# Kernel tuning notes

Measured on AMD Instinct MI355X. Metric: run time of the kernel, lower is better.

Reference implementation:

```python
import jax, jax.numpy as jnp
import numpy as np
from jax import lax

B, C, H, W = 8, 512, 48, 48
E = 512          # embed_dim (== in_channels, required by GLoR fusion channel math)
P = 128          # ContextBlock planes = int(512*0.25)
NC = 2           # num_classes; also used (buggily, but faithfully) as BGAM threshold
TOPK_RATIO = 0.1


def conv1x1(x, w, b=None):
    # w: [out, in]
    y = jnp.einsum('bchw,oc->bohw', x, w)
    if b is not None:
        y = y + b[None, :, None, None]
    return y


def conv3x3(x, w, b):
    y = lax.conv_general_dilated(x, w, (1, 1), 'SAME',
                                 dimension_numbers=('NCHW', 'OIHW', 'NCHW'))
    return y + b[None, :, None, None]


def dwconv3x3(x, w):
    # depthwise: w [C,1,3,3], feature_group_count=C
    return lax.conv_general_dilated(x, w, (1, 1), 'SAME',
                                    dimension_numbers=('NCHW', 'OIHW', 'NCHW'),
                                    feature_group_count=x.shape[1])


def bn_eval(x, g, b):
    # eval-mode BatchNorm2d, running_mean=0, running_var=1, eps=1e-5
    scale = g / jnp.sqrt(1.0 + 1e-5)
    return x * scale[None, :, None, None] + b[None, :, None, None]


def chan_mlp(c, w1, b1, g, bl, w2, b2):
    # ContextBlock channel transform: 1x1 conv -> LayerNorm([P,1,1]) -> ReLU -> 1x1 conv, on [B,C] vectors
    h = c @ w1.T + b1                                  # [B,P]
    mu = h.mean(-1, keepdims=True)
    var = jnp.var(h, axis=-1, keepdims=True)
    h = (h - mu) / jnp.sqrt(var + 1e-5) * g + bl
    h = jax.nn.relu(h)
    return h @ w2.T + b2                               # [B,C]


def cos_self(t):
    # torch F.cosine_similarity(t, t, dim=1): dot/(max(n,eps)*max(n,eps)), eps=1e-8
    nrm2 = jnp.sum(t * t, axis=1)                      # [B,H,W]
    n = jnp.maximum(jnp.sqrt(nrm2), 1e-8)
    return nrm2 / (n * n)


def setup_inputs() -> dict:
    key = jax.random.key(0)
    ks = iter(jax.random.split(key, 64))
    def nrm(shape, scale):
        return (jax.random.normal(next(ks), shape) * scale).astype(jnp.float32)
    def gma(n):
        return (1.0 + 0.05 * jax.random.normal(next(ks), (n,))).astype(jnp.float32)
    def bta(n):
        return (0.05 * jax.random.normal(next(ks), (n,))).astype(jnp.float32)
    sC = 1.0 / np.sqrt(C)
    return dict(
        x=jax.random.normal(next(ks), (B, C, H, W), jnp.float32),
        # GLoR local ConvBranch
        lb_w1=nrm((E, C), sC), lb_g1=gma(E), lb_b1=bta(E),
        lb_w2=nrm((E, 1, 3, 3), 1.0 / 3.0), lb_g2=gma(E), lb_b2=bta(E),
        lb_w3=nrm((E, E), 1.0 / np.sqrt(E)), lb_g3=gma(E), lb_b3=bta(E),
        # GLoR ContextBlock (att pooling, channel_add + channel_mul)
        cm_w=nrm((1, C), sC), cm_b=bta(1),
        ca_w1=nrm((P, C), sC), ca_b1=bta(P), ca_lg=gma(P), ca_lb=bta(P),
        ca_w2=nrm((C, P), 1.0 / np.sqrt(P)), ca_b2=bta(C),
        cmu_w1=nrm((P, C), sC), cmu_b1=bta(P), cmu_lg=gma(P), cmu_lb=bta(P),
        cmu_w2=nrm((C, P), 1.0 / np.sqrt(P)), cmu_b2=bta(C),
        fu_w=nrm((E, 2 * E), 1.0 / np.sqrt(2 * E)), fu_b=bta(E),
        # heads
        sh_w=nrm((NC, E), 1.0 / np.sqrt(E)), sh_b=bta(NC),
        bh_w=nrm((2, E), 1.0 / np.sqrt(E)), bh_b=bta(2),
        # ReverseAttention
        ra_w1=nrm((2, 2, 3, 3), 1.0 / np.sqrt(18)), ra_b1=bta(2), ra_g1=gma(2), ra_bb1=bta(2),
        ra_w2=nrm((2, 2, 3, 3), 1.0 / np.sqrt(18)), ra_b2=bta(2), ra_g2=gma(2), ra_bb2=bta(2),
        # AGCR (all bias=False)
        q_w=nrm((E // 4, E), 1.0 / np.sqrt(E)), k_w=nrm((E // 4, E), 1.0 / np.sqrt(E)),
        v_w=nrm((E, E), 1.0 / np.sqrt(E)), fin_w=nrm((E, 2 * E), 1.0 / np.sqrt(2 * E)),
    )


def reference(x, lb_w1, lb_g1, lb_b1, lb_w2, lb_g2, lb_b2, lb_w3, lb_g3, lb_b3,
              cm_w, cm_b, ca_w1, ca_b1, ca_lg, ca_lb, ca_w2, ca_b2,
              cmu_w1, cmu_b1, cmu_lg, cmu_lb, cmu_w2, cmu_b2, fu_w, fu_b,
              sh_w, sh_b, bh_w, bh_b,
              ra_w1, ra_b1, ra_g1, ra_bb1, ra_w2, ra_b2, ra_g2, ra_bb2,
              q_w, k_w, v_w, fin_w):
    b_, c_, h_, w_ = x.shape
    N = h_ * w_
    # ---- GLoR: local ConvBranch ----
    t = jax.nn.relu(bn_eval(conv1x1(x, lb_w1), lb_g1, lb_b1))
    t = jax.nn.relu(bn_eval(dwconv3x3(t, lb_w2), lb_g2, lb_b2))
    local = bn_eval(conv1x1(t, lb_w3), lb_g3, lb_b3)
    # ---- GLoR: ContextBlock (att pooling) ----
    xf = x.reshape(b_, c_, N)
    mask = (conv1x1(x, cm_w, cm_b)).reshape(b_, 1, N)
    mask = jax.nn.softmax(mask, axis=2)
    ctx = jnp.einsum('bcn,bn->bc', xf, mask[:, 0, :])              # [B,C]
    mul = jax.nn.sigmoid(chan_mlp(ctx, cmu_w1, cmu_b1, cmu_lg, cmu_lb, cmu_w2, cmu_b2))
    add = chan_mlp(ctx, ca_w1, ca_b1, ca_lg, ca_lb, ca_w2, ca_b2)
    glob = x * mul[:, :, None, None] + add[:, :, None, None]
    gx = conv1x1(jnp.concatenate([local, glob], axis=1), fu_w, fu_b)  # [B,E,H,W]
    # ---- heads ----
    sem = conv1x1(gx, sh_w, sh_b)                                   # [B,NC,H,W]
    bdl = conv1x1(gx, bh_w, bh_b)                                   # [B,2,H,W]
    # ---- ReverseAttention(boundary_logits, sigmoid(boundary_logits)) ----
    wx = bdl * (1.0 - jax.nn.sigmoid(bdl))
    r = jax.nn.relu(bn_eval(conv3x3(wx, ra_w1, ra_b1), ra_g1, ra_bb1))
    r = jax.nn.relu(bn_eval(conv3x3(r, ra_w2, ra_b2), ra_g2, ra_bb2))
    # ---- BGAM (threshold = num_classes, faithful to source) ----
    thr = jnp.float32(NC)
    st = (cos_self(sem) > thr).astype(x.dtype)
    bt = (cos_self(r) > thr).astype(x.dtype)
    region = ((1.0 - st) * (1.0 - bt))[:, None]                     # [B,1,H,W]
    # ---- AGCR custom attention ----
    k_num = int(N * TOPK_RATIO)
    q = conv1x1(gx, q_w).reshape(b_, -1, N)                         # [B,E/4,N]
    kk = conv1x1(gx, k_w).reshape(b_, -1, N)
    v = conv1x1(gx, v_w).reshape(b_, E, N)
    attn = jnp.einsum('bdm,bdn->bmn', q, kk) / jnp.sqrt(jnp.float32(q.shape[1]))
    aw = jax.nn.softmax(attn, axis=-1)                              # [B,N,N]
    topv, _ = lax.top_k(aw, k_num)
    soft = topv.mean(-1)                                            # [B,N]
    aw = aw * soft[:, None, :]
    # bmm(value, aw^T).mean(-1) == value @ aw.mean(rows)
    col_mean = aw.mean(axis=1)                                      # [B,N]
    ctx2 = jnp.einsum('bcn,bn->bc', v, col_mean)                    # [B,E]
    ctx2 = jnp.broadcast_to(ctx2[:, :, None, None], gx.shape)
    refined = jnp.concatenate([gx, ctx2 * region], axis=1)          # [B,2E,H,W]
    return conv1x1(refined, fin_w)                                  # [B,E,H,W]
```

## Files before the change

### kernel.cpp

```cpp
#include <hip/hip_runtime.h>
#include <math.h>

#define NPIX 2304
#define NCH  512
#define NB   8
#define KNUM 230

typedef unsigned short u16;
typedef __attribute__((ext_vector_type(8))) short short8v;
typedef __attribute__((ext_vector_type(4))) float float4v;

__device__ __forceinline__ float bf2f(u16 u) {
    union { unsigned v; float f; } x; x.v = ((unsigned)u) << 16; return x.f;
}
__device__ __forceinline__ u16 f2bf(float f) {
    union { float f; unsigned v; } x; x.f = f;
    unsigned r = x.v + 0x7FFFu + ((x.v >> 16) & 1u);
    return (u16)(r >> 16);
}

__device__ __forceinline__ float waveSum(float v) {
    #pragma unroll
    for (int o = 32; o > 0; o >>= 1) v += __shfl_down(v, o);
    return v;
}
__device__ __forceinline__ float blockSum256(float v, float* sc4) {
    v = waveSum(v);
    __syncthreads();
    if ((threadIdx.x & 63) == 0) sc4[threadIdx.x >> 6] = v;
    __syncthreads();
    return sc4[0] + sc4[1] + sc4[2] + sc4[3];
}
__device__ __forceinline__ float waveMaxF(float v) {
    #pragma unroll
    for (int o = 32; o > 0; o >>= 1) v = fmaxf(v, __shfl_down(v, o));
    return v;
}
__device__ __forceinline__ float blockMax256(float v, float* sc4) {
    v = waveMaxF(v);
    __syncthreads();
    if ((threadIdx.x & 63) == 0) sc4[threadIdx.x >> 6] = v;
    __syncthreads();
    return fmaxf(fmaxf(sc4[0], sc4[1]), fmaxf(sc4[2], sc4[3]));
}

__device__ __forceinline__ void gl_lds16(const u16* g, u16* l) {
    __builtin_amdgcn_global_load_lds(
        reinterpret_cast<const unsigned __attribute__((address_space(1)))*>(
            reinterpret_cast<uintptr_t>(g)),
        reinterpret_cast<unsigned __attribute__((address_space(3)))*>(
            reinterpret_cast<uintptr_t>(l)),
        16, 0, 0);
}

__global__ __launch_bounds__(256, 3) void mfma_gemm(
    const u16* __restrict__ A, int ldA, long sA,
    const u16* __restrict__ B0, const u16* __restrict__ B1, int ldB, long sB,
    void* __restrict__ outp, int ldO, long sO,
    const float* __restrict__ scaleR, const float* __restrict__ biasR,
    const float* __restrict__ biasC, int ldbc,
    const float* __restrict__ biasRB, int ldrb,
    int K, float alpha, int flags)
{
    __shared__ u16 lA[128 * 64];
    __shared__ u16 lB[128 * 64];
    const int t  = threadIdx.x;
    const int w  = t >> 6, l = t & 63;
    const int wR = w >> 1, wC = w & 1;
    const int lg = l >> 4, lr = l & 15, l7 = l & 7;
    const int b   = blockIdx.z;
    const int Cl0 = blockIdx.x * 128;
    const int R0  = blockIdx.y * 128;
    const u16* Ab  = A + (size_t)b * sA;
    const u16* B0b = B0 + (size_t)b * sB;
    const u16* B1b = B1 ? B1 + (size_t)b * sB : nullptr;

    float4v acc[4][4];
    const float4v zero = {0.f, 0.f, 0.f, 0.f};
    #pragma unroll
    for (int i = 0; i < 4; ++i)
        #pragma unroll
        for (int j = 0; j < 4; ++j) acc[i][j] = zero;

    const int sr = t >> 3;
    const int sp = t & 7;

    for (int k0 = 0; k0 < K; k0 += 64) {
        const u16* Bsrc = B0b; int kb = k0;
        if (B1b && k0 >= 512) { Bsrc = B1b; kb = k0 - 512; }
        #pragma unroll
        for (int i = 0; i < 4; ++i) {
            const int r  = i * 32 + sr;
            const int ca = sp ^ (r & 7);
            gl_lds16(Ab   + (size_t)(R0  + r) * ldA + (k0 + ca * 8), &lA[i * 2048 + t * 8]);
            gl_lds16(Bsrc + (size_t)(Cl0 + r) * ldB + (kb + ca * 8), &lB[i * 2048 + t * 8]);
        }
        __syncthreads();
        #pragma unroll
        for (int kk = 0; kk < 2; ++kk) {
            short8v af[4], bfv[4];
            const int p = (kk * 4 + lg) ^ l7;
            #pragma unroll
            for (int mt = 0; mt < 4; ++mt) {
                const int rA = wR * 64 + mt * 16 + lr;
                af[mt]  = *reinterpret_cast<const short8v*>(&lA[rA * 64 + p * 8]);
                const int rB = wC * 64 + mt * 16 + lr;
                bfv[mt] = *reinterpret_cast<const short8v*>(&lB[rB * 64 + p * 8]);
            }
            #pragma unroll
            for (int mt = 0; mt < 4; ++mt)
                #pragma unroll
                for (int nt = 0; nt < 4; ++nt)
                    acc[mt][nt] = __builtin_amdgcn_mfma_f32_16x16x32_bf16(
                        af[mt], bfv[nt], acc[mt][nt], 0, 0, 0);
        }
        __syncthreads();
    }

    const bool relu = (flags & 1), f32o = (flags & 2);
    #pragma unroll
    for (int nt = 0; nt < 4; ++nt) {
        const int Cl = Cl0 + wC * 64 + nt * 16 + lr;
        const float bc = biasC ? biasC[(size_t)b * ldbc + Cl] : 0.f;
        #pragma unroll
        for (int mt = 0; mt < 4; ++mt) {
            const int Rb = R0 + wR * 64 + mt * 16 + lg * 4;
            float4 scv = scaleR ? *reinterpret_cast<const float4*>(&scaleR[Rb])
                                : make_float4(1.f, 1.f, 1.f, 1.f);
            float4 bv  = biasR  ? *reinterpret_cast<const float4*>(&biasR[Rb])
                                : make_float4(0.f, 0.f, 0.f, 0.f);
            float4 rbv = biasRB ? *reinterpret_cast<const float4*>(&biasRB[(size_t)b * ldrb + Rb])
                                : make_float4(0.f, 0.f, 0.f, 0.f);
            float vals[4];
            #pragma unroll
            for (int j = 0; j < 4; ++j) {
                const float sc = alpha * ((&scv.x)[j]);
                float v = acc[mt][nt][j] * sc + (&bv.x)[j] + bc + (&rbv.x)[j];
                if (relu) v = fmaxf(v, 0.f);
                vals[j] = v;
            }
            if (f32o) {
                float* op = (float*)outp + (size_t)b * sO + (size_t)Cl * ldO + Rb;
                *reinterpret_cast<float4*>(op) = make_float4(vals[0], vals[1], vals[2], vals[3]);
            } else {
                ushort4 u;
                u.x = f2bf(vals[0]); u.y = f2bf(vals[1]);
                u.z = f2bf(vals[2]); u.w = f2bf(vals[3]);
                u16* op = (u16*)outp + (size_t)b * sO + (size_t)Cl * ldO + Rb;
                *reinterpret_cast<ushort4*>(op) = u;
            }
        }
    }
}

__global__ __launch_bounds__(256) void transpose_cvt_ml(
    const float* __restrict__ x, const float* __restrict__ cmw,
    u16* __restrict__ xb, float* __restrict__ logits)
{
    __shared__ float tile[64][65];
    const int t = threadIdx.x;
    const int n0 = blockIdx.x * 64, c0 = blockIdx.y * 64, b = blockIdx.z;
    const int tr = t >> 4, tc4 = (t & 15) * 4;
    #pragma unroll
    for (int i = 0; i < 4; ++i) {
        const int cc = tr + i * 16;
        float4 v = *reinterpret_cast<const float4*>(
            x + ((size_t)(b * NCH + c0 + cc)) * NPIX + n0 + tc4);
        tile[cc][tc4 + 0] = v.x; tile[cc][tc4 + 1] = v.y;
        tile[cc][tc4 + 2] = v.z; tile[cc][tc4 + 3] = v.w;
    }
    __syncthreads();
    #pragma unroll
    for (int i = 0; i < 4; ++i) {
        const int nn = tr + i * 16;
        ushort4 u;
        u.x = f2bf(tile[tc4 + 0][nn]); u.y = f2bf(tile[tc4 + 1][nn]);
        u.z = f2bf(tile[tc4 + 2][nn]); u.w = f2bf(tile[tc4 + 3][nn]);
        *reinterpret_cast<ushort4*>(xb + ((size_t)b * NPIX + n0 + nn) * NCH + c0 + tc4) = u;
    }
    const int nl = t >> 2, q = t & 3;
    float s = 0.f;
    #pragma unroll
    for (int k = 0; k < 16; ++k) {
        const int cc = q * 16 + k;
        s = fmaf(tile[cc][nl], cmw[c0 + cc], s);
    }
    s += __shfl_xor(s, 1);
    s += __shfl_xor(s, 2);
    if (q == 0) atomicAdd(&logits[(size_t)b * NPIX + n0 + nl], s);
}

__global__ __launch_bounds__(256) void transpose_w3(
    const float* __restrict__ w3, const float* __restrict__ g3, u16* __restrict__ w3t)
{
    __shared__ float tile[64][65];
    const int t = threadIdx.x;
    const int k0 = blockIdx.x * 64, c0 = blockIdx.y * 64;
    const int tr = t >> 4, tc4 = (t & 15) * 4;
    #pragma unroll
    for (int i = 0; i < 4; ++i) {
        const int cc = tr + i * 16;
        const float s = g3[c0 + cc] * 0.99999500003749978f;
        float4 v = *reinterpret_cast<const float4*>(&w3[(size_t)(c0 + cc) * 512 + k0 + tc4]);
        tile[cc][tc4 + 0] = v.x * s; tile[cc][tc4 + 1] = v.y * s;
        tile[cc][tc4 + 2] = v.z * s; tile[cc][tc4 + 3] = v.w * s;
    }
    __syncthreads();
    #pragma unroll
    for (int i = 0; i < 4; ++i) {
        const int kk = tr + i * 16;
        ushort4 u;
        u.x = f2bf(tile[tc4 + 0][kk]); u.y = f2bf(tile[tc4 + 1][kk]);
        u.z = f2bf(tile[tc4 + 2][kk]); u.w = f2bf(tile[tc4 + 3][kk]);
        *reinterpret_cast<ushort4*>(&w3t[(size_t)(k0 + kk) * 512 + c0 + tc4]) = u;
    }
}

__device__ __forceinline__ void cvt4(const float* s, u16* d, int i) {
    float4 v = reinterpret_cast<const float4*>(s)[i];
    ushort4 u; u.x = f2bf(v.x); u.y = f2bf(v.y); u.z = f2bf(v.z); u.w = f2bf(v.w);
    reinterpret_cast<ushort4*>(d)[i] = u;
}
__global__ __launch_bounds__(256) void prep_weights(
    const float* __restrict__ w1, const float* __restrict__ fu,
    const float* __restrict__ fin, const float* __restrict__ qw,
    const float* __restrict__ kw, const float* __restrict__ vw,
    const float* __restrict__ dww, const float* __restrict__ dwg,
    u16* __restrict__ w1b, u16* __restrict__ fuwb, u16* __restrict__ finwb,
    u16* __restrict__ qkvwb, float* __restrict__ wfold)
{
    const int i = blockIdx.x * 256 + threadIdx.x;
    if (i < 65536)            cvt4(w1, w1b, i);
    else if (i < 196608)      cvt4(fu, fuwb, i - 65536);
    else if (i < 327680)      cvt4(fin, finwb, i - 196608);
    else if (i < 344064)      cvt4(qw, qkvwb, i - 327680);
    else if (i < 360448)      cvt4(kw, qkvwb + 128 * 512, i - 344064);
    else if (i < 425984)      cvt4(vw, qkvwb + 256 * 512, i - 360448);
    else if (i < 425984 + 4608) {
        const int j = i - 425984;
        const int c = j / 9, tap = j % 9;
        wfold[tap * NCH + c] = dww[j] * dwg[c] * 0.99999500003749978f;
    }
}

__global__ __launch_bounds__(256) void dwconv_k(
    const u16* __restrict__ t1, const float* __restrict__ wf,
    const float* __restrict__ b2, u16* __restrict__ t2)
{
    const int idx = blockIdx.x * 256 + threadIdx.x;
    const int cq = idx & 127;
    const int n  = (idx >> 7) % NPIX;
    const int b  = (idx >> 7) / NPIX;
    const int c  = cq * 4;
    const int y = n / 48, x = n % 48;
    float s0 = 0.f, s1 = 0.f, s2 = 0.f, s3 = 0.f;
    #pragma unroll
    for (int dy = -1; dy <= 1; ++dy) {
        const int yy = y + dy;
        if (yy < 0 || yy >= 48) continue;
        #pragma unroll
        for (int dx = -1; dx <= 1; ++dx) {
            const int xx = x + dx;
            if (xx < 0 || xx >= 48) continue;
            ushort4 tv = *reinterpret_cast<const ushort4*>(
                &t1[((size_t)b * NPIX + yy * 48 + xx) * NCH + c]);
            float4 wv = *reinterpret_cast<const float4*>(
                &wf[((dy + 1) * 3 + dx + 1) * NCH + c]);
            s0 = fmaf(bf2f(tv.x), wv.x, s0); s1 = fmaf(bf2f(tv.y), wv.y, s1);
            s2 = fmaf(bf2f(tv.z), wv.z, s2); s3 = fmaf(bf2f(tv.w), wv.w, s3);
        }
    }
    float4 bb = *reinterpret_cast<const float4*>(&b2[c]);
    ushort4 o;
    o.x = f2bf(fmaxf(s0 + bb.x, 0.f)); o.y = f2bf(fmaxf(s1 + bb.y, 0.f));
    o.z = f2bf(fmaxf(s2 + bb.z, 0.f)); o.w = f2bf(fmaxf(s3 + bb.w, 0.f));
    *reinterpret_cast<ushort4*>(&t2[((size_t)b * NPIX + n) * NCH + c]) = o;
}

__global__ __launch_bounds__(256) void softmax_mask(
    const float* __restrict__ logits, float* __restrict__ mask)
{
    __shared__ float sc[4];
    const int b = blockIdx.x, t = threadIdx.x;
    const float* lr = logits + (size_t)b * NPIX;
    float mx = -3.4e38f;
    for (int i = t; i < NPIX; i += 256) mx = fmaxf(mx, lr[i]);
    mx = blockMax256(mx, sc);
    float s = 0.f;
    for (int i = t; i < NPIX; i += 256) s += __expf(lr[i] - mx);
    s = blockSum256(s, sc);
    const float inv = 1.0f / s;
    for (int i = t; i < NPIX; i += 256) mask[(size_t)b * NPIX + i] = __expf(lr[i] - mx) * inv;
}

__global__ __launch_bounds__(512) void ctx_pool_k(
    const u16* __restrict__ xb, const float* __restrict__ mask, float* __restrict__ ctx)
{
    const int c = threadIdx.x, b = blockIdx.y;
    const int nn0 = blockIdx.x * 128;
    float s = 0.f;
    for (int n = nn0; n < nn0 + 128; ++n)
        s = fmaf(bf2f(xb[((size_t)b * NPIX + n) * NCH + c]), mask[(size_t)b * NPIX + n], s);
    atomicAdd(&ctx[b * NCH + c], s);
}

__global__ __launch_bounds__(256) void chan_h(
    const float* __restrict__ ctxv,
    const float* __restrict__ mw1, const float* __restrict__ mb1,
    const float* __restrict__ aw1, const float* __restrict__ ab1,
    float* __restrict__ hnb)
{
    const int w = threadIdx.x >> 6, l = threadIdx.x & 63;
    const int gid = blockIdx.x * 4 + w;
    const int path = gid >> 10;
    const int rem  = gid & 1023;
    const int h = rem >> 3, b = rem & 7;
    const float* W1 = path ? aw1 : mw1;
    const float* B1 = path ? ab1 : mb1;
    const float4 wa = *reinterpret_cast<const float4*>(&W1[h * 512 + l * 8]);
    const float4 wb = *reinterpret_cast<const float4*>(&W1[h * 512 + l * 8 + 4]);
    const float4 ca = *reinterpret_cast<const float4*>(&ctxv[b * 512 + l * 8]);
    const float4 cb = *reinterpret_cast<const float4*>(&ctxv[b * 512 + l * 8 + 4]);
    float s = wa.x * ca.x + wa.y * ca.y + wa.z * ca.z + wa.w * ca.w
            + wb.x * cb.x + wb.y * cb.y + wb.z * cb.z + wb.w * cb.w;
    s = waveSum(s);
    if (l == 0) hnb[(path * 8 + b) * 128 + h] = s + B1[h];
}

__global__ __launch_bounds__(128) void chan_ln(
    const float* __restrict__ mlg, const float* __restrict__ mlb,
    const float* __restrict__ alg, const float* __restrict__ alb,
    float* __restrict__ hnb)
{
    __shared__ float sc[2];
    const int path = blockIdx.x, b = blockIdx.y, t = threadIdx.x;
    float* hp = hnb + (path * 8 + b) * 128;
    const float v = hp[t];
    float s1 = waveSum(v);
    if ((t & 63) == 0) sc[t >> 6] = s1;
    __syncthreads();
    const float mu = (sc[0] + sc[1]) * (1.0f / 128.0f);
    const float d = v - mu;
    float s2 = waveSum(d * d);
    __syncthreads();
    if ((t & 63) == 0) sc[t >> 6] = s2;
    __syncthreads();
    const float var = (sc[0] + sc[1]) * (1.0f / 128.0f);
    const float* LG = path ? alg : mlg;
    const float* LB = path ? alb : mlb;
    hp[t] = fmaxf(d / sqrtf(var + 1e-5f) * LG[t] + LB[t], 0.f);
}

__global__ __launch_bounds__(128) void chan_o(
    const float* __restrict__ hnb,
    const float* __restrict__ mw2, const float* __restrict__ mb2,
    const float* __restrict__ aw2, const float* __restrict__ ab2,
    float* __restrict__ mulo, float* __restrict__ addo)
{
    __shared__ float hs[128];
    const int oc = blockIdx.x, path = blockIdx.y, b = blockIdx.z;
    const int t = threadIdx.x;
    hs[t] = hnb[(path * 8 + b) * 128 + t];
    __syncthreads();
    const int o = oc * 128 + t;
    const float* W2 = path ? aw2 : mw2;
    float s = (path ? ab2 : mb2)[o];
    #pragma unroll
    for (int p = 0; p < 128; p += 4) {
        const float4 wv = *reinterpret_cast<const float4*>(&W2[o * 128 + p]);
        s += wv.x * hs[p] + wv.y * hs[p + 1] + wv.z * hs[p + 2] + wv.w * hs[p + 3];
    }
    if (path == 0) mulo[b * 512 + o] = 1.0f / (1.0f + __expf(-s));
    else           addo[b * 512 + o] = s;
}

__global__ __launch_bounds__(256) void scale_wglob(
    const float* __restrict__ fuw, const float* __restrict__ mulv, u16* __restrict__ wf)
{
    const int idx = blockIdx.x * 256 + threadIdx.x;
    const int cq = idx & 127;
    const int o  = (idx >> 7) & 511;
    const int b  = idx >> 16;
    const int c  = cq * 4;
    float4 w = *reinterpret_cast<const float4*>(&fuw[(size_t)o * 1024 + 512 + c]);
    float4 m = *reinterpret_cast<const float4*>(&mulv[b * 512 + c]);
    ushort4 u;
    u.x = f2bf(w.x * m.x); u.y = f2bf(w.y * m.y);
    u.z = f2bf(w.z * m.z); u.w = f2bf(w.w * m.w);
    *reinterpret_cast<ushort4*>(&wf[(size_t)b * 524288 + (size_t)o * 1024 + 512 + c]) = u;
}

__global__ __launch_bounds__(256) void fuse_bias(
    const float* __restrict__ fuw, const float* __restrict__ fub,
    const float* __restrict__ b3, const float* __restrict__ addv, float* __restrict__ fb)
{
    const int o = blockIdx.x * 256 + threadIdx.x;
    const int b = blockIdx.y;
    const float* wr = fuw + (size_t)o * 1024;
    float s = fub[o];
    for (int c = 0; c < 512; c += 4) {
        float4 w1 = *reinterpret_cast<const float4*>(&wr[c]);
        float4 bv = *reinterpret_cast<const float4*>(&b3[c]);
        float4 w2 = *reinterpret_cast<const float4*>(&wr[512 + c]);
        float4 av = *reinterpret_cast<const float4*>(&addv[b * 512 + c]);
        s += w1.x * bv.x + w1.y * bv.y + w1.z * bv.z + w1.w * bv.w
           + w2.x * av.x + w2.y * av.y + w2.z * av.z + w2.w * av.w;
    }
    fb[b * 512 + o] = s;
}

__global__ __launch_bounds__(256) void softmax_topk_wave(
    const u16* __restrict__ p, float* __restrict__ mxo,
    float* __restrict__ invSo, float* __restrict__ softo)
{
    const int w = threadIdx.x >> 6, l = threadIdx.x & 63;
    const int r = blockIdx.x * 4 + w;
    const int bc = blockIdx.y;
    const u16* pr = p + ((size_t)bc * NPIX + r) * NPIX;
    const uint4* p16 = reinterpret_cast<const uint4*>(pr);
    uint4 q0 = p16[l], q1 = p16[64 + l], q2 = p16[128 + l], q3 = p16[192 + l];
    uint2 q4 = reinterpret_cast<const uint2*>(pr)[512 + l];
    unsigned uw[18] = {q0.x, q0.y, q0.z, q0.w, q1.x, q1.y, q1.z, q1.w,
                       q2.x, q2.y, q2.z, q2.w, q3.x, q3.y, q3.z, q3.w,
                       q4.x, q4.y};
    unsigned km[36];
    #pragma unroll
    for (int i = 0; i < 18; ++i) {
        const unsigned v = uw[i];
        const unsigned m = ((v >> 15) & 0x10001u) * 0x7FFFu + 0x80008000u;
        const unsigned s = v ^ m;
        km[2 * i]     = s & 0xFFFFu;
        km[2 * i + 1] = s >> 16;
    }
    unsigned kmax = km[0];
    #pragma unroll
    for (int i = 1; i < 36; ++i) kmax = max(kmax, km[i]);
    #pragma unroll
    for (int o = 32; o > 0; o >>= 1) kmax = max(kmax, (unsigned)__shfl_xor((int)kmax, o));
    const unsigned mxbits = (kmax & 0x8000u) ? (kmax ^ 0x8000u) : (kmax ^ 0xFFFFu);
    const float mx = bf2f((u16)mxbits);
    unsigned kt = 0u;
    for (int bit = 15; bit >= 0; --bit) {
        const unsigned cand = kt | (1u << bit);
        int c = 0;
        #pragma unroll
        for (int i = 0; i < 36; ++i)
            c += (int)__popcll(__ballot(km[i] >= cand));
        if (c >= KNUM) kt = cand;
    }
    const unsigned tbits = (kt & 0x8000u) ? (kt ^ 0x8000u) : (kt ^ 0xFFFFu);
    const float te = __expf(bf2f((u16)tbits) - mx);
    float S = 0.f, ss = 0.f; int a = 0;
    #pragma unroll
    for (int i = 0; i < 36; ++i) {
        const unsigned bb = (km[i] & 0x8000u) ? (km[i] ^ 0x8000u) : (km[i] ^ 0xFFFFu);
        const float e = __expf(bf2f((u16)bb) - mx);
        S += e;
        const bool gt = km[i] > kt;
        if (gt) ss += e;
        a += (int)__popcll(__ballot(gt));
    }
    #pragma unroll
    for (int o = 32; o > 0; o >>= 1) { S += __shfl_xor(S, o); ss += __shfl_xor(ss, o); }
    if (l == 0) {
        const size_t gi = (size_t)bc * NPIX + r;
        mxo[gi] = mx; invSo[gi] = 1.0f / S;
        softo[gi] = (ss + (float)(KNUM - a) * te) / (S * (float)KNUM);
    }
}

__global__ __launch_bounds__(256) void colsum_k(
    const u16* __restrict__ p, const float* __restrict__ mxo,
    const float* __restrict__ invSo, float* __restrict__ colsum)
{
    const int j = blockIdx.x * 256 + threadIdx.x;
    const int ic0 = blockIdx.y * 72;
    const int bc = blockIdx.z;
    const float* mxr = mxo + (size_t)bc * NPIX;
    const float* isr = invSo + (size_t)bc * NPIX;
    const u16* pb = p + (size_t)bc * NPIX * NPIX;
    float s = 0.f;
    #pragma unroll 4
    for (int i = ic0; i < ic0 + 72; ++i)
        s += __expf(bf2f(pb[(size_t)i * NPIX + j]) - mxr[i]) * isr[i];
    atomicAdd(&colsum[(size_t)bc * NPIX + j], s);
}

__global__ __launch_bounds__(512) void ctx2_pool_k(
    const u16* __restrict__ qkv, const float* __restrict__ colsum,
    const float* __restrict__ soft, float* __restrict__ ctx2)
{
    const int c = threadIdx.x, b = blockIdx.y;
    const int nn0 = blockIdx.x * 128;
    float s = 0.f;
    for (int n = nn0; n < nn0 + 128; ++n) {
        const float wgt = colsum[(size_t)b * NPIX + n] * soft[(size_t)b * NPIX + n];
        s = fmaf(bf2f(qkv[((size_t)b * NPIX + n) * 768 + 256 + c]), wgt, s);
    }
    atomicAdd(&ctx2[b * NCH + c], s * (1.0f / (float)NPIX));
}

__global__ __launch_bounds__(256) void compute_z(
    const float* __restrict__ finw, const float* __restrict__ ctx2, float* __restrict__ z)
{
    const int o = blockIdx.x * 256 + threadIdx.x;
    const int b = blockIdx.y;
    const float* c2 = ctx2 + b * NCH;
    const float* wr = finw + (size_t)o * 1024 + 512;
    float s = 0.f;
    for (int c = 0; c < NCH; ++c) s = fmaf(wr[c], c2[c], s);
    z[b * NCH + o] = s;
}

extern "C" void kernel_launch(void* const* d_in, const int* in_sizes, int n_in,
                              void* d_out, int out_size, void* d_ws, size_t ws_size,
                              hipStream_t stream)
{
    (void)in_sizes; (void)n_in; (void)out_size; (void)ws_size;
    const float* x      = (const float*)d_in[0];
    const float* lb_w1  = (const float*)d_in[1];
    const float* lb_g1  = (const float*)d_in[2];
    const float* lb_b1  = (const float*)d_in[3];
    const float* lb_w2  = (const float*)d_in[4];
    const float* lb_g2  = (const float*)d_in[5];
    const float* lb_b2  = (const float*)d_in[6];
    const float* lb_w3  = (const float*)d_in[7];
    const float* lb_g3  = (const float*)d_in[8];
    const float* lb_b3  = (const float*)d_in[9];
    const float* cm_w   = (const float*)d_in[10];
    const float* ca_w1  = (const float*)d_in[12];
    const float* ca_b1  = (const float*)d_in[13];
    const float* ca_lg  = (const float*)d_in[14];
    const float* ca_lb  = (const float*)d_in[15];
    const float* ca_w2  = (const float*)d_in[16];
    const float* ca_b2  = (const float*)d_in[17];
    const float* cmu_w1 = (const float*)d_in[18];
    const float* cmu_b1 = (const float*)d_in[19];
    const float* cmu_lg = (const float*)d_in[20];
    const float* cmu_lb = (const float*)d_in[21];
    const float* cmu_w2 = (const float*)d_in[22];
    const float* cmu_b2 = (const float*)d_in[23];
    const float* fu_w   = (const float*)d_in[24];
    const float* fu_b   = (const float*)d_in[25];
    const float* q_w    = (const float*)d_in[38];
    const float* k_w    = (const float*)d_in[39];
    const float* v_w    = (const float*)d_in[40];
    const float* fin_w  = (const float*)d_in[41];

    char* W = (char*)d_ws;
    const size_t SZ_ACT = (size_t)NB * NPIX * NCH * 2;
    u16* xb   = (u16*)(W);
    u16* bufA = (u16*)(W + SZ_ACT);
    u16* bufB = (u16*)(W + 2 * SZ_ACT);
    u16* gx   = (u16*)(W + 3 * SZ_ACT);
    u16* qkv  = (u16*)(W + 4 * SZ_ACT);
    u16* wfused = qkv;
    u16* pbuf = (u16*)(W + 4 * SZ_ACT + (size_t)NB * NPIX * 768 * 2);
    char* SM = (char*)(pbuf + (size_t)NB * NPIX * NPIX);
    float* logits = (float*)SM; SM += (size_t)NB * NPIX * 4;
    float* colsum = (float*)SM; SM += (size_t)NB * NPIX * 4;
    float* ctxb   = (float*)SM; SM += (size_t)NB * NCH * 4;
    float* ctx2b  = (float*)SM; SM += (size_t)NB * NCH * 4;
    float* maskb  = (float*)SM; SM += (size_t)NB * NPIX * 4;
    float* mxb    = (float*)SM; SM += (size_t)NB * NPIX * 4;
    float* invSb  = (float*)SM; SM += (size_t)NB * NPIX * 4;
    float* softb  = (float*)SM; SM += (size_t)NB * NPIX * 4;
    float* mulb   = (float*)SM; SM += (size_t)NB * NCH * 4;
    float* addb   = (float*)SM; SM += (size_t)NB * NCH * 4;
    float* zbuf   = (float*)SM; SM += (size_t)NB * NCH * 4;
    float* fbias  = (float*)SM; SM += (size_t)NB * NCH * 4;
    float* hnb    = (float*)SM; SM += (size_t)2 * NB * 128 * 4;
    float* wfold  = (float*)SM; SM += (size_t)9 * NCH * 4;
    u16* w1b   = (u16*)SM; SM += (size_t)512 * 512 * 2;
    u16* fuwb  = (u16*)SM; SM += (size_t)512 * 1024 * 2;
    u16* finwb = (u16*)SM; SM += (size_t)512 * 1024 * 2;
    u16* qkvwb = (u16*)SM; SM += (size_t)768 * 512 * 2;
    u16* w3t   = (u16*)SM; SM += (size_t)512 * 512 * 2;

    const float invs  = 0.99999500003749978f;
    const float rs128 = 0.08838834764831845f;
    const long SACT = (long)NPIX * NCH;

    hipMemsetAsync(logits, 0,
        ((size_t)2 * NB * NPIX + (size_t)2 * NB * NCH) * 4, stream);
    prep_weights<<<1683, 256, 0, stream>>>(lb_w1, fu_w, fin_w, q_w, k_w, v_w,
        lb_w2, lb_g2, w1b, fuwb, finwb, qkvwb, wfold);
    transpose_cvt_ml<<<dim3(36, 8, 8), 256, 0, stream>>>(x, cm_w, xb, logits);
    transpose_w3<<<dim3(8, 8), 256, 0, stream>>>(lb_w3, lb_g3, w3t);

    mfma_gemm<<<dim3(4, 4, 8), 256, 0, stream>>>(w3t, 512, 0, fuwb, nullptr, 1024, 0,
        wfused, 1024, 524288, nullptr, nullptr, nullptr, 0, nullptr, 0, 512, 1.0f, 0);

    mfma_gemm<<<dim3(18, 4, 8), 256, 0, stream>>>(w1b, 512, 0, xb, nullptr, 512, SACT,
        bufA, 512, SACT, lb_g1, lb_b1, nullptr, 0, nullptr, 0, 512, invs, 1);
    dwconv_k<<<9216, 256, 0, stream>>>(bufA, wfold, lb_b2, bufB);
    softmax_mask<<<8, 256, 0, stream>>>(logits, maskb);
    ctx_pool_k<<<dim3(18, 8), 512, 0, stream>>>(xb, maskb, ctxb);
    chan_h<<<512, 256, 0, stream>>>(ctxb, cmu_w1, cmu_b1, ca_w1, ca_b1, hnb);
    chan_ln<<<dim3(2, 8), 128, 0, stream>>>(cmu_lg, cmu_lb, ca_lg, ca_lb, hnb);
    chan_o<<<dim3(4, 2, 8), 128, 0, stream>>>(hnb, cmu_w2, cmu_b2, ca_w2, ca_b2, mulb, addb);
    scale_wglob<<<2048, 256, 0, stream>>>(fu_w, mulb, wfused);
    fuse_bias<<<dim3(2, 8), 256, 0, stream>>>(fu_w, fu_b, lb_b3, addb, fbias);
    mfma_gemm<<<dim3(18, 4, 8), 256, 0, stream>>>(wfused, 1024, 524288, bufB, xb, 512, SACT,
        gx, 512, SACT, nullptr, nullptr, nullptr, 0, fbias, 512, 1024, 1.0f, 0);
    mfma_gemm<<<dim3(18, 6, 8), 256, 0, stream>>>(qkvwb, 512, 0, gx, nullptr, 512, SACT,
        qkv, 768, (long)NPIX * 768, nullptr, nullptr, nullptr, 0, nullptr, 0, 512, 1.0f, 0);
    mfma_gemm<<<dim3(18, 18, 8), 256, 0, stream>>>(qkv + 128, 768, (long)NPIX * 768,
        qkv, nullptr, 768, (long)NPIX * 768,
        pbuf, NPIX, (long)NPIX * NPIX, nullptr, nullptr, nullptr, 0, nullptr, 0,
        128, rs128, 0);
    softmax_topk_wave<<<dim3(576, 8), 256, 0, stream>>>(pbuf, mxb, invSb, softb);
    colsum_k<<<dim3(9, 32, 8), 256, 0, stream>>>(pbuf, mxb, invSb, colsum);
    ctx2_pool_k<<<dim3(18, 8), 512, 0, stream>>>(qkv, colsum, softb, ctx2b);
    compute_z<<<dim3(2, 8), 256, 0, stream>>>(fin_w, ctx2b, zbuf);
    mfma_gemm<<<dim3(4, 18, 8), 256, 0, stream>>>(gx, 512, SACT, finwb, nullptr, 1024, 0,
        d_out, NPIX, (long)NCH * NPIX, nullptr, nullptr, zbuf, 512, nullptr, 0,
        512, 1.0f, 2);
}
```

Before: 386.2 us.

## Fuse QK^T GEMM, softmax top-k and column sum into one LDS-resident kernel

Replaces the separate attention-score GEMM, the per-row softmax/top-k kernel and the column-sum kernel with one kernel. Each block computes a 16-row strip of scores with MFMA into shared memory, does the per-row max, top-k threshold and softmax statistics from LDS, then accumulates column sums with atomics. This removes the write and two re-reads of the full 8x2304x2304 bf16 score matrix in global memory and its workspace buffer. In exchange each block reloads K for the whole row strip from global/L2, uses about 74KB of LDS (limiting occupancy), and issues more atomics on colsum (144 contributions per column instead of 32).

New measurement: 467.2 us. 21.0% more time.

```diff
diff --git a/kernel.cpp b/kernel.cpp
--- a/kernel.cpp
+++ b/kernel.cpp
@@ -5,6 +5,7 @@
 #define NCH  512
 #define NB   8
 #define KNUM 230
+#define SROW 2312
 
 typedef unsigned short u16;
 typedef __attribute__((ext_vector_type(8))) short short8v;
@@ -409,81 +410,108 @@
     fb[b * 512 + o] = s;
 }
 
-__global__ __launch_bounds__(256) void softmax_topk_wave(
-    const u16* __restrict__ p, float* __restrict__ mxo,
-    float* __restrict__ invSo, float* __restrict__ softo)
-{
-    const int w = threadIdx.x >> 6, l = threadIdx.x & 63;
-    const int r = blockIdx.x * 4 + w;
-    const int bc = blockIdx.y;
-    const u16* pr = p + ((size_t)bc * NPIX + r) * NPIX;
-    const uint4* p16 = reinterpret_cast<const uint4*>(pr);
-    uint4 q0 = p16[l], q1 = p16[64 + l], q2 = p16[128 + l], q3 = p16[192 + l];
-    uint2 q4 = reinterpret_cast<const uint2*>(pr)[512 + l];
-    unsigned uw[18] = {q0.x, q0.y, q0.z, q0.w, q1.x, q1.y, q1.z, q1.w,
-                       q2.x, q2.y, q2.z, q2.w, q3.x, q3.y, q3.z, q3.w,
-                       q4.x, q4.y};
-    unsigned km[36];
-    #pragma unroll
-    for (int i = 0; i < 18; ++i) {
-        const unsigned v = uw[i];
-        const unsigned m = ((v >> 15) & 0x10001u) * 0x7FFFu + 0x80008000u;
-        const unsigned s = v ^ m;
-        km[2 * i]     = s & 0xFFFFu;
-        km[2 * i + 1] = s >> 16;
-    }
-    unsigned kmax = km[0];
-    #pragma unroll
-    for (int i = 1; i < 36; ++i) kmax = max(kmax, km[i]);
-    #pragma unroll
-    for (int o = 32; o > 0; o >>= 1) kmax = max(kmax, (unsigned)__shfl_xor((int)kmax, o));
-    const unsigned mxbits = (kmax & 0x8000u) ? (kmax ^ 0x8000u) : (kmax ^ 0xFFFFu);
-    const float mx = bf2f((u16)mxbits);
-    unsigned kt = 0u;
-    for (int bit = 15; bit >= 0; --bit) {
-        const unsigned cand = kt | (1u << bit);
-        int c = 0;
-        #pragma unroll
-        for (int i = 0; i < 36; ++i)
-            c += (int)__popcll(__ballot(km[i] >= cand));
-        if (c >= KNUM) kt = cand;
-    }
-    const unsigned tbits = (kt & 0x8000u) ? (kt ^ 0x8000u) : (kt ^ 0xFFFFu);
-    const float te = __expf(bf2f((u16)tbits) - mx);
-    float S = 0.f, ss = 0.f; int a = 0;
-    #pragma unroll
-    for (int i = 0; i < 36; ++i) {
-        const unsigned bb = (km[i] & 0x8000u) ? (km[i] ^ 0x8000u) : (km[i] ^ 0xFFFFu);
-        const float e = __expf(bf2f((u16)bb) - mx);
-        S += e;
-        const bool gt = km[i] > kt;
-        if (gt) ss += e;
-        a += (int)__popcll(__ballot(gt));
-    }
-    #pragma unroll
-    for (int o = 32; o > 0; o >>= 1) { S += __shfl_xor(S, o); ss += __shfl_xor(ss, o); }
-    if (l == 0) {
-        const size_t gi = (size_t)bc * NPIX + r;
-        mxo[gi] = mx; invSo[gi] = 1.0f / S;
-        softo[gi] = (ss + (float)(KNUM - a) * te) / (S * (float)KNUM);
-    }
-}
-
-__global__ __launch_bounds__(256) void colsum_k(
-    const u16* __restrict__ p, const float* __restrict__ mxo,
-    const float* __restrict__ invSo, float* __restrict__ colsum)
-{
-    const int j = blockIdx.x * 256 + threadIdx.x;
-    const int ic0 = blockIdx.y * 72;
-    const int bc = blockIdx.z;
-    const float* mxr = mxo + (size_t)bc * NPIX;
-    const float* isr = invSo + (size_t)bc * NPIX;
-    const u16* pb = p + (size_t)bc * NPIX * NPIX;
-    float s = 0.f;
-    #pragma unroll 4
-    for (int i = ic0; i < ic0 + 72; ++i)
-        s += __expf(bf2f(pb[(size_t)i * NPIX + j]) - mxr[i]) * isr[i];
-    atomicAdd(&colsum[(size_t)bc * NPIX + j], s);
+__global__ __launch_bounds__(256) void fused_attn(
+    const u16* __restrict__ qkv, float* __restrict__ colsum,
+    float* __restrict__ softo, float alpha)
+{
+    __shared__ u16 S[16][SROW];
+    __shared__ float rowmx[16], rowinv[16];
+    const int t = threadIdx.x;
+    const int w = t >> 6, l = t & 63;
+    const int lr = l & 15, lg = l >> 4;
+    const int m0 = blockIdx.x * 16;
+    const int b  = blockIdx.y;
+    const u16* qb = qkv + (size_t)b * NPIX * 768;
+
+    short8v qf[4];
+    #pragma unroll
+    for (int kk = 0; kk < 4; ++kk)
+        qf[kk] = *reinterpret_cast<const short8v*>(qb + (size_t)(m0 + lr) * 768 + kk * 32 + lg * 8);
+
+    const float4v zero = {0.f, 0.f, 0.f, 0.f};
+    for (int ct = w; ct < 144; ct += 4) {
+        const int n0 = ct * 16;
+        float4v acc = zero;
+        #pragma unroll
+        for (int kk = 0; kk < 4; ++kk) {
+            const short8v kf = *reinterpret_cast<const short8v*>(
+                qb + (size_t)(n0 + lr) * 768 + 128 + kk * 32 + lg * 8);
+            acc = __builtin_amdgcn_mfma_f32_16x16x32_bf16(kf, qf[kk], acc, 0, 0, 0);
+        }
+        ushort4 u;
+        u.x = f2bf(acc[0] * alpha); u.y = f2bf(acc[1] * alpha);
+        u.z = f2bf(acc[2] * alpha); u.w = f2bf(acc[3] * alpha);
+        *reinterpret_cast<ushort4*>(&S[lr][n0 + lg * 4]) = u;
+    }
+    __syncthreads();
+
+    for (int rr = 0; rr < 4; ++rr) {
+        const int mrow = w * 4 + rr;
+        const u16* pr = &S[mrow][0];
+        const uint4* p16 = reinterpret_cast<const uint4*>(pr);
+        uint4 q0 = p16[l], q1 = p16[64 + l], q2 = p16[128 + l], q3 = p16[192 + l];
+        uint2 q4 = reinterpret_cast<const uint2*>(pr)[512 + l];
+        unsigned uw[18] = {q0.x, q0.y, q0.z, q0.w, q1.x, q1.y, q1.z, q1.w,
+                           q2.x, q2.y, q2.z, q2.w, q3.x, q3.y, q3.z, q3.w,
+                           q4.x, q4.y};
+        unsigned km[36];
+        #pragma unroll
+        for (int i = 0; i < 18; ++i) {
+            const unsigned v = uw[i];
+            const unsigned m = ((v >> 15) & 0x10001u) * 0x7FFFu + 0x80008000u;
+            const unsigned s = v ^ m;
+            km[2 * i]     = s & 0xFFFFu;
+            km[2 * i + 1] = s >> 16;
+        }
+        unsigned kmax = km[0];
+        #pragma unroll
+        for (int i = 1; i < 36; ++i) kmax = max(kmax, km[i]);
+        #pragma unroll
+        for (int o = 32; o > 0; o >>= 1) kmax = max(kmax, (unsigned)__shfl_xor((int)kmax, o));
+        const unsigned mxbits = (kmax & 0x8000u) ? (kmax ^ 0x8000u) : (kmax ^ 0xFFFFu);
+        const float mx = bf2f((u16)mxbits);
+        unsigned kt = 0u;
+        for (int bit = 15; bit >= 0; --bit) {
+            const unsigned cand = kt | (1u << bit);
+            int c = 0;
+            #pragma unroll
+            for (int i = 0; i < 36; ++i)
+                c += (int)__popcll(__ballot(km[i] >= cand));
+            if (c >= KNUM) kt = cand;
+        }
+        const unsigned tbits = (kt & 0x8000u) ? (kt ^ 0x8000u) : (kt ^ 0xFFFFu);
+        const float te = __expf(bf2f((u16)tbits) - mx);
+        float Ssum = 0.f, ss = 0.f; int a = 0;
+        #pragma unroll
+        for (int i = 0; i < 36; ++i) {
+            const unsigned bb = (km[i] & 0x8000u) ? (km[i] ^ 0x8000u) : (km[i] ^ 0xFFFFu);
+            const float e = __expf(bf2f((u16)bb) - mx);
+            Ssum += e;
+            const bool gt = km[i] > kt;
+            if (gt) ss += e;
+            a += (int)__popcll(__ballot(gt));
+        }
+        #pragma unroll
+        for (int o = 32; o > 0; o >>= 1) { Ssum += __shfl_xor(Ssum, o); ss += __shfl_xor(ss, o); }
+        if (l == 0) {
+            const float invS = 1.0f / Ssum;
+            rowmx[mrow] = mx; rowinv[mrow] = invS;
+            softo[(size_t)b * NPIX + m0 + mrow] =
+                (ss + (float)(KNUM - a) * te) * invS * (1.0f / (float)KNUM);
+        }
+    }
+    __syncthreads();
+
+    float rm[16], ri[16];
+    #pragma unroll
+    for (int i = 0; i < 16; ++i) { rm[i] = rowmx[i]; ri[i] = rowinv[i]; }
+    for (int j = t; j < NPIX; j += 256) {
+        float s = 0.f;
+        #pragma unroll
+        for (int i = 0; i < 16; ++i)
+            s = fmaf(__expf(bf2f(S[i][j]) - rm[i]), ri[i], s);
+        atomicAdd(&colsum[(size_t)b * NPIX + j], s);
+    }
 }
 
 __global__ __launch_bounds__(512) void ctx2_pool_k(
@@ -555,15 +583,12 @@
     u16* gx   = (u16*)(W + 3 * SZ_ACT);
     u16* qkv  = (u16*)(W + 4 * SZ_ACT);
     u16* wfused = qkv;
-    u16* pbuf = (u16*)(W + 4 * SZ_ACT + (size_t)NB * NPIX * 768 * 2);
-    char* SM = (char*)(pbuf + (size_t)NB * NPIX * NPIX);
+    char* SM = (char*)(qkv + (size_t)NB * NPIX * 768);
     float* logits = (float*)SM; SM += (size_t)NB * NPIX * 4;
     float* colsum = (float*)SM; SM += (size_t)NB * NPIX * 4;
     float* ctxb   = (float*)SM; SM += (size_t)NB * NCH * 4;
     float* ctx2b  = (float*)SM; SM += (size_t)NB * NCH * 4;
     float* maskb  = (float*)SM; SM += (size_t)NB * NPIX * 4;
-    float* mxb    = (float*)SM; SM += (size_t)NB * NPIX * 4;
-    float* invSb  = (float*)SM; SM += (size_t)NB * NPIX * 4;
     float* softb  = (float*)SM; SM += (size_t)NB * NPIX * 4;
     float* mulb   = (float*)SM; SM += (size_t)NB * NCH * 4;
     float* addb   = (float*)SM; SM += (size_t)NB * NCH * 4;
@@ -605,12 +630,7 @@
         gx, 512, SACT, nullptr, nullptr, nullptr, 0, fbias, 512, 1024, 1.0f, 0);
     mfma_gemm<<<dim3(18, 6, 8), 256, 0, stream>>>(qkvwb, 512, 0, gx, nullptr, 512, SACT,
         qkv, 768, (long)NPIX * 768, nullptr, nullptr, nullptr, 0, nullptr, 0, 512, 1.0f, 0);
-    mfma_gemm<<<dim3(18, 18, 8), 256, 0, stream>>>(qkv + 128, 768, (long)NPIX * 768,
-        qkv, nullptr, 768, (long)NPIX * 768,
-        pbuf, NPIX, (long)NPIX * NPIX, nullptr, nullptr, nullptr, 0, nullptr, 0,
-        128, rs128, 0);
-    softmax_topk_wave<<<dim3(576, 8), 256, 0, stream>>>(pbuf, mxb, invSb, softb);
-    colsum_k<<<dim3(9, 32, 8), 256, 0, stream>>>(pbuf, mxb, invSb, colsum);
+    fused_attn<<<dim3(144, 8), 256, 0, stream>>>(qkv, colsum, softb, rs128);
     ctx2_pool_k<<<dim3(18, 8), 512, 0, stream>>>(qkv, colsum, softb, ctx2b);
     compute_z<<<dim3(2, 8), 256, 0, stream>>>(fin_w, ctx2b, zbuf);
     mfma_gemm<<<dim3(4, 18, 8), 256, 0, stream>>>(gx, 512, SACT, finwb, nullptr, 1024, 0,
```
